# Kernel tuning notes

Measured on AMD Instinct MI355X. Metric: run time of the kernel, lower is better.

Reference implementation:

```python
import jax, jax.numpy as jnp
import numpy as np

B, C, D, O = 64, 64, 512, 256
N_REG, G = 8, 8  # 8 regions of 8 channels


def setup_inputs() -> dict:
    key = jax.random.key(0)
    ks = jax.random.split(key, 9)
    std = 0.02  # init_weights_classify: normal(0, 0.02) for Linear weights, zero bias
    x = jax.random.normal(ks[0], (B, C, D), dtype=jnp.float32)
    region_indices = jnp.arange(C, dtype=jnp.int32).reshape(N_REG, G)
    # attn_fc: Linear(2D -> D), ReLU, Linear(D -> 1)
    W1 = jax.random.normal(ks[1], (2 * D, D), dtype=jnp.float32) * std
    b1 = jnp.zeros((D,), jnp.float32)
    W2 = jax.random.normal(ks[2], (D, 1), dtype=jnp.float32) * std
    b2 = jnp.zeros((1,), jnp.float32)
    # gcn1: Linear(D -> D); gcn2: Linear(D -> O)
    Wg1 = jax.random.normal(ks[3], (D, D), dtype=jnp.float32) * std
    bg1 = jnp.zeros((D,), jnp.float32)
    Wg2 = jax.random.normal(ks[4], (D, O), dtype=jnp.float32) * std
    bg2 = jnp.zeros((O,), jnp.float32)
    return {"x": x, "W1": W1, "b1": b1, "W2": W2, "b2": b2,
            "Wg1": Wg1, "bg1": bg1, "Wg2": Wg2, "bg2": bg2,
            "region_indices": region_indices}


def _leaky_relu02(z):
    return jnp.where(z >= 0, z, 0.2 * z)


def reference(x, W1, b1, W2, b2, Wg1, bg1, Wg2, bg2, region_indices):
    Bb, Cc, Dd = x.shape
    n_reg, g = region_indices.shape
    # channel -> region id; mask[i,j] = same region and i != j
    rid = jnp.zeros((Cc,), jnp.int32).at[region_indices.reshape(-1)].set(
        jnp.repeat(jnp.arange(n_reg, dtype=jnp.int32), g))
    idx = jnp.arange(Cc)
    mask = (rid[:, None] == rid[None, :]) & (idx[:, None] != idx[None, :])  # [C, C]
    # attn_fc on cat(x_i, x_j): split first linear to avoid [B,C,C,2D] concat
    a = x @ W1[:Dd]   # [B, C, D]
    bpart = x @ W1[Dd:]  # [B, C, D]
    h = jax.nn.relu(a[:, :, None, :] + bpart[:, None, :, :] + b1)  # [B, C, C, D]
    scores = jnp.einsum('bijd,do->bij', h, W2) + b2[0]  # [B, C, C]
    scores = jnp.where(mask[None, :, :], scores, -jnp.inf)
    adj = jax.nn.softmax(scores, axis=-1)  # [B, C, C]
    # gcn1: adj @ x -> Linear -> LeakyReLU(0.2); residual mix
    m1 = jnp.einsum('bij,bjd->bid', adj, x)
    x1 = _leaky_relu02(m1 @ Wg1 + bg1)
    x1 = 0.5 * x1 + 0.5 * x
    # gcn2
    m2 = jnp.einsum('bij,bjd->bid', adj, x1)
    out = _leaky_relu02(m2 @ Wg2 + bg2)  # [B, C, O]
    return out
```

## Files before the change

### kernel.cpp

```cpp
#include <hip/hip_runtime.h>
#include <math.h>

#define B_   64
#define C_   64
#define D_   512
#define O_   256
#define G_   8
#define M_   4096

typedef __attribute__((ext_vector_type(8))) short s16x8;
typedef __attribute__((ext_vector_type(4))) float f32x4;
typedef unsigned short u16;
typedef unsigned int   u32;

__device__ __forceinline__ float bf2f(u16 u) { return __uint_as_float(((u32)u) << 16); }
__device__ __forceinline__ u16 f2bf(float f) {
    u32 u = __float_as_uint(f);
    return (u16)((u + 0x7FFFu + ((u >> 16) & 1u)) >> 16);
}
__device__ __forceinline__ void gload16(const void* g, void* l) {
    __builtin_amdgcn_global_load_lds((const __attribute__((address_space(1))) u32*)g,
                                     (__attribute__((address_space(3))) u32*)l, 16, 0, 0);
}
__device__ __forceinline__ void xcd_swz(int& bx, int& by) {
    int nx = (int)gridDim.x;
    int L = bx + by * nx;
    int nwg = nx * (int)gridDim.y;
    int nid = (L & 7) * (nwg >> 3) + (L >> 3);
    bx = nid & (nx - 1);
    by = nid / nx;
}

__global__ __launch_bounds__(256)
void prep_kernel(const float* __restrict__ x, u16* __restrict__ x_bf,
                 const float* __restrict__ W1, u16* __restrict__ W1t,
                 const float* __restrict__ Wg1, u16* __restrict__ Wg1t,
                 const float* __restrict__ Wg2, u16* __restrict__ Wg2t)
{
    __shared__ float tile[32][33];
    const int bx = blockIdx.x, tid = threadIdx.x;
    if (bx < 1024) {
        size_t i = ((size_t)bx * 256 + tid) * 8;
        const float4* p = (const float4*)(x + i);
        float4 v0 = p[0], v1 = p[1];
        s16x8 o;
        o[0] = (short)f2bf(v0.x); o[1] = (short)f2bf(v0.y);
        o[2] = (short)f2bf(v0.z); o[3] = (short)f2bf(v0.w);
        o[4] = (short)f2bf(v1.x); o[5] = (short)f2bf(v1.y);
        o[6] = (short)f2bf(v1.z); o[7] = (short)f2bf(v1.w);
        *(s16x8*)(x_bf + i) = o;
        return;
    }
    const float* src; u16* dst; int k0, n0, nsrc, obase;
    if (bx < 1536) {
        int idx = bx - 1024, h = idx >> 8, t = idx & 255;
        src = W1 + (size_t)h * 512 * 512; dst = W1t; obase = h * 512;
        k0 = (t >> 4) * 32; n0 = (t & 15) * 32; nsrc = 512;
    } else if (bx < 1792) {
        int t = bx - 1536;
        src = Wg1; dst = Wg1t; obase = 0;
        k0 = (t >> 4) * 32; n0 = (t & 15) * 32; nsrc = 512;
    } else {
        int t = bx - 1792;
        src = Wg2; dst = Wg2t; obase = 0;
        k0 = (t >> 3) * 32; n0 = (t & 7) * 32; nsrc = 256;
    }
    int tx = tid & 31, ty = tid >> 5;
    #pragma unroll
    for (int j = 0; j < 4; j++)
        tile[ty + j * 8][tx] = src[(size_t)(k0 + ty + j * 8) * nsrc + n0 + tx];
    __syncthreads();
    #pragma unroll
    for (int j = 0; j < 4; j++)
        dst[(size_t)(obase + n0 + ty + j * 8) * 512 + k0 + tx] = f2bf(tile[tx][ty + j * 8]);
}

__global__ __launch_bounds__(512)
void gemm1_kernel(const u16* __restrict__ A, const u16* __restrict__ Bt,
                  u16* __restrict__ Obf0, u16* __restrict__ Obf1)
{
    constexpr int K = 512, BK = 64, NT = K / BK;
    __shared__ __align__(16) u16 As[2][128 * 64];
    __shared__ __align__(16) u16 Bs[2][128 * 64];

    const int tid = threadIdx.x;
    const int lane = tid & 63;
    const int w = tid >> 6;
    const int wr = w >> 1, wc = w & 1;
    const int lr = lane & 15, lq = lane >> 4;
    int bx = blockIdx.x, by = blockIdx.y;
    xcd_swz(bx, by);
    const int m0 = by * 128, n0 = bx * 128;

    const int sr = tid >> 3;
    const int ss = tid & 7;
    const int gsl = ss ^ (sr & 7);

    f32x4 acc[2][4] = {};

    auto stage = [&](int buf, int kt) {
        #pragma unroll
        for (int ch = 0; ch < 2; ch++)
            gload16(A + (size_t)(m0 + ch * 64 + sr) * K + kt + gsl * 8,
                    &As[buf][ch * 4096 + tid * 8]);
        #pragma unroll
        for (int ch = 0; ch < 2; ch++)
            gload16(Bt + (size_t)(n0 + ch * 64 + sr) * K + kt + gsl * 8,
                    &Bs[buf][ch * 4096 + tid * 8]);
    };

    stage(0, 0);
    int cur = 0;
    for (int t = 0; t < NT; t++) {
        __syncthreads();
        if (t + 1 < NT) stage(cur ^ 1, (t + 1) * BK);
        const u16* as = As[cur]; const u16* bs = Bs[cur];
        #pragma unroll
        for (int ks = 0; ks < 2; ks++) {
            s16x8 af[2], bfv[4];
            #pragma unroll
            for (int m = 0; m < 2; m++) {
                int r = wr * 32 + m * 16 + lr;
                af[m] = *(const s16x8*)(as + r * 64 + (((ks * 4 + lq) ^ (r & 7)) * 8));
            }
            #pragma unroll
            for (int n = 0; n < 4; n++) {
                int r = wc * 64 + n * 16 + lr;
                bfv[n] = *(const s16x8*)(bs + r * 64 + (((ks * 4 + lq) ^ (r & 7)) * 8));
            }
            #pragma unroll
            for (int m = 0; m < 2; m++)
                #pragma unroll
                for (int n = 0; n < 4; n++)
                    acc[m][n] = __builtin_amdgcn_mfma_f32_16x16x32_bf16(af[m], bfv[n], acc[m][n], 0, 0, 0);
        }
        cur ^= 1;
    }

    #pragma unroll
    for (int m = 0; m < 2; m++) {
        #pragma unroll
        for (int n = 0; n < 4; n++) {
            #pragma unroll
            for (int j = 0; j < 4; j++) {
                int row = m0 + wr * 32 + m * 16 + lq * 4 + j;
                int col = n0 + wc * 64 + n * 16 + lr;
                float v = acc[m][n][j];
                if (col < 512) Obf0[(size_t)row * 512 + col] = f2bf(v);
                else           Obf1[(size_t)row * 512 + col - 512] = f2bf(v);
            }
        }
    }
}

__global__ __launch_bounds__(256)
void scores_m1_kernel(const u16* __restrict__ a_bf, const u16* __restrict__ bp_bf,
                      const u16* __restrict__ x_bf,
                      const float* __restrict__ b1, const float* __restrict__ W2,
                      const float* __restrict__ b2,
                      const int* __restrict__ region_indices,
                      float* __restrict__ adjw, u16* __restrict__ m1)
{
    __shared__ __align__(16) u16 bp_lds[64 * 512];
    __shared__ int ri_lds[64];
    __shared__ int rid_lds[64];

    int L = blockIdx.x;
    int nid = ((L & 7) << 5) + (L >> 3);
    const int b = nid >> 2, q = nid & 3;
    const int tid = threadIdx.x, lane = tid & 63, w = tid >> 6;

    #pragma unroll
    for (int it = 0; it < 16; it++)
        gload16(bp_bf + (size_t)b * 32768 + it * 2048 + tid * 8, bp_lds + it * 2048 + tid * 8);
    if (tid < 64) {
        int c = region_indices[tid];
        ri_lds[tid] = c;
        rid_lds[c] = tid >> 3;
    }

    const int d0 = lane * 8;
    float4 b1a = *(const float4*)(b1 + d0), b1b = *(const float4*)(b1 + d0 + 4);
    float4 w2a = *(const float4*)(W2 + d0), w2b = *(const float4*)(W2 + d0 + 4);
    float b1v[8] = { b1a.x, b1a.y, b1a.z, b1a.w, b1b.x, b1b.y, b1b.z, b1b.w };
    float w2v[8] = { w2a.x, w2a.y, w2a.z, w2a.w, w2b.x, w2b.y, w2b.z, w2b.w };
    const float bias2 = b2[0];

    __syncthreads();

    for (int rr = 0; rr < 4; rr++) {
        const int i = q * 16 + w * 4 + rr;
        const int bi = b * 64 + i;
        const int r = rid_lds[i];
        int mem[8];
        #pragma unroll
        for (int m = 0; m < 8; m++) mem[m] = ri_lds[r * 8 + m];

        s16x8 a8 = *(const s16x8*)(a_bf + (size_t)bi * 512 + d0);
        float ai[8];
        #pragma unroll
        for (int t = 0; t < 8; t++) ai[t] = bf2f((u16)a8[t]) + b1v[t];

        float p[8];
        #pragma unroll
        for (int m = 0; m < 8; m++) {
            s16x8 bv = *(const s16x8*)(bp_lds + mem[m] * 512 + d0);
            float s = 0.f;
            #pragma unroll
            for (int t = 0; t < 8; t++) {
                float h = ai[t] + bf2f((u16)bv[t]);
                s += fmaxf(h, 0.f) * w2v[t];
            }
            p[m] = s;
        }
        #pragma unroll
        for (int off = 32; off >= 1; off >>= 1)
            #pragma unroll
            for (int m = 0; m < 8; m++) p[m] += __shfl_xor(p[m], off);

        float scmax = -INFINITY;
        #pragma unroll
        for (int m = 0; m < 8; m++) {
            p[m] = (mem[m] == i) ? -INFINITY : p[m] + bias2;
            scmax = fmaxf(scmax, p[m]);
        }
        float esum = 0.f;
        #pragma unroll
        for (int m = 0; m < 8; m++) {
            p[m] = (mem[m] == i) ? 0.f : __expf(p[m] - scmax);
            esum += p[m];
        }
        const float inv = 1.f / esum;

        float accv[8] = {};
        #pragma unroll
        for (int m = 0; m < 8; m++) {
            p[m] *= inv;
            s16x8 xv = *(const s16x8*)(x_bf + ((size_t)(b * 64 + mem[m])) * 512 + d0);
            #pragma unroll
            for (int t = 0; t < 8; t++) accv[t] += p[m] * bf2f((u16)xv[t]);
        }
        s16x8 o;
        #pragma unroll
        for (int t = 0; t < 8; t++) o[t] = (short)f2bf(accv[t]);
        *(s16x8*)(m1 + (size_t)bi * 512 + d0) = o;
        if (lane < 8) adjw[(size_t)bi * 8 + lane] = p[lane];
    }
}

__global__ __launch_bounds__(512)
void gemm2_m2_kernel(const u16* __restrict__ A, const u16* __restrict__ Bt,
                     const float* __restrict__ bias, const float* __restrict__ xres,
                     const float* __restrict__ adjw, const int* __restrict__ region_indices,
                     u16* __restrict__ m2)
{
    constexpr int K = 512, BK = 64, NT = K / BK;
    __shared__ __align__(16) u16 As[2][64 * 64];
    __shared__ __align__(16) u16 Bs[2][128 * 64];
    __shared__ __align__(16) u16 x1s[64 * 136];
    __shared__ int ri_lds[64];
    __shared__ int rid_lds[64];

    const int tid = threadIdx.x;
    const int lane = tid & 63;
    const int w = tid >> 6;
    const int wr = w >> 2, wc = w & 3;
    const int lr = lane & 15, lq = lane >> 4;
    int bx = blockIdx.x, by = blockIdx.y;
    xcd_swz(bx, by);
    const int b = by, n0 = bx * 128, m0 = b * 64;

    const int sr = tid >> 3, ss = tid & 7;
    const int gsl = ss ^ (sr & 7);

    if (tid < 64) {
        int c = region_indices[tid];
        ri_lds[tid] = c;
        rid_lds[c] = tid >> 3;
    }

    f32x4 acc[2][2] = {};

    auto stage = [&](int buf, int kt) {
        gload16(A + (size_t)(m0 + sr) * K + kt + gsl * 8, &As[buf][tid * 8]);
        #pragma unroll
        for (int ch = 0; ch < 2; ch++)
            gload16(Bt + (size_t)(n0 + ch * 64 + sr) * K + kt + gsl * 8,
                    &Bs[buf][ch * 4096 + tid * 8]);
    };

    stage(0, 0);
    int cur = 0;
    for (int t = 0; t < NT; t++) {
        __syncthreads();
        if (t + 1 < NT) stage(cur ^ 1, (t + 1) * BK);
        const u16* as = As[cur]; const u16* bs = Bs[cur];
        #pragma unroll
        for (int ks = 0; ks < 2; ks++) {
            s16x8 af[2], bfv[2];
            #pragma unroll
            for (int m = 0; m < 2; m++) {
                int r = wr * 32 + m * 16 + lr;
                af[m] = *(const s16x8*)(as + r * 64 + (((ks * 4 + lq) ^ (r & 7)) * 8));
            }
            #pragma unroll
            for (int n = 0; n < 2; n++) {
                int r = wc * 32 + n * 16 + lr;
                bfv[n] = *(const s16x8*)(bs + r * 64 + (((ks * 4 + lq) ^ (r & 7)) * 8));
            }
            #pragma unroll
            for (int m = 0; m < 2; m++)
                #pragma unroll
                for (int n = 0; n < 2; n++)
                    acc[m][n] = __builtin_amdgcn_mfma_f32_16x16x32_bf16(af[m], bfv[n], acc[m][n], 0, 0, 0);
        }
        cur ^= 1;
    }

    #pragma unroll
    for (int m = 0; m < 2; m++) {
        #pragma unroll
        for (int n = 0; n < 2; n++) {
            #pragma unroll
            for (int j = 0; j < 4; j++) {
                int lrow = wr * 32 + m * 16 + lq * 4 + j;
                int lcol = wc * 32 + n * 16 + lr;
                float v = acc[m][n][j] + bias[n0 + lcol];
                v = (v >= 0.f) ? v : 0.2f * v;
                v = 0.5f * v + 0.5f * xres[(size_t)(m0 + lrow) * 512 + n0 + lcol];
                x1s[lrow * 136 + lcol] = f2bf(v);
            }
        }
    }
    __syncthreads();

    const int i = tid >> 3, cb = tid & 7, c0 = cb * 16;
    const int bi = m0 + i;
    const int r = rid_lds[i];
    float acc2[16] = {};
    #pragma unroll
    for (int m = 0; m < 8; m++) {
        float wm = adjw[(size_t)bi * 8 + m];
        int j = ri_lds[r * 8 + m];
        #pragma unroll
        for (int cc = 0; cc < 2; cc++) {
            s16x8 v = *(const s16x8*)(x1s + j * 136 + c0 + cc * 8);
            #pragma unroll
            for (int t = 0; t < 8; t++) acc2[cc * 8 + t] += wm * bf2f((u16)v[t]);
        }
    }
    #pragma unroll
    for (int cc = 0; cc < 2; cc++) {
        s16x8 o;
        #pragma unroll
        for (int t = 0; t < 8; t++) o[t] = (short)f2bf(acc2[cc * 8 + t]);
        *(s16x8*)(m2 + (size_t)bi * 512 + n0 + c0 + cc * 8) = o;
    }
}

__global__ __launch_bounds__(256)
void gemm3_kernel(const u16* __restrict__ A, const u16* __restrict__ Bt,
                  const float* __restrict__ bias, float* __restrict__ Of)
{
    constexpr int K = 512, BK = 64, NT = K / BK;
    __shared__ __align__(16) u16 As[2][64 * 64];
    __shared__ __align__(16) u16 Bs[2][64 * 64];

    const int tid = threadIdx.x;
    const int lane = tid & 63;
    const int w = tid >> 6, wr = w >> 1, wc = w & 1;
    const int lr = lane & 15, lq = lane >> 4;
    int bx = blockIdx.x, by = blockIdx.y;
    xcd_swz(bx, by);
    const int m0 = by * 64, n0 = bx * 64;

    const int sr = tid >> 3, ss = tid & 7;
    const int gsl = ss ^ (sr & 7);

    f32x4 acc[2][2] = {};

    auto stage = [&](int buf, int kt) {
        #pragma unroll
        for (int ch = 0; ch < 2; ch++)
            gload16(A + (size_t)(m0 + ch * 32 + sr) * K + kt + gsl * 8,
                    &As[buf][ch * 2048 + tid * 8]);
        #pragma unroll
        for (int ch = 0; ch < 2; ch++)
            gload16(Bt + (size_t)(n0 + ch * 32 + sr) * K + kt + gsl * 8,
                    &Bs[buf][ch * 2048 + tid * 8]);
    };

    stage(0, 0);
    int cur = 0;
    for (int t = 0; t < NT; t++) {
        __syncthreads();
        if (t + 1 < NT) stage(cur ^ 1, (t + 1) * BK);
        const u16* as = As[cur]; const u16* bs = Bs[cur];
        #pragma unroll
        for (int ks = 0; ks < 2; ks++) {
            s16x8 af[2], bfv[2];
            #pragma unroll
            for (int m = 0; m < 2; m++) {
                int r = wr * 32 + m * 16 + lr;
                af[m] = *(const s16x8*)(as + r * 64 + (((ks * 4 + lq) ^ (r & 7)) * 8));
            }
            #pragma unroll
            for (int n = 0; n < 2; n++) {
                int r = wc * 32 + n * 16 + lr;
                bfv[n] = *(const s16x8*)(bs + r * 64 + (((ks * 4 + lq) ^ (r & 7)) * 8));
            }
            #pragma unroll
            for (int m = 0; m < 2; m++)
                #pragma unroll
                for (int n = 0; n < 2; n++)
                    acc[m][n] = __builtin_amdgcn_mfma_f32_16x16x32_bf16(af[m], bfv[n], acc[m][n], 0, 0, 0);
        }
        cur ^= 1;
    }

    #pragma unroll
    for (int m = 0; m < 2; m++) {
        #pragma unroll
        for (int n = 0; n < 2; n++) {
            #pragma unroll
            for (int j = 0; j < 4; j++) {
                int row = m0 + wr * 32 + m * 16 + lq * 4 + j;
                int col = n0 + wc * 32 + n * 16 + lr;
                float v = acc[m][n][j] + bias[col];
                v = (v >= 0.f) ? v : 0.2f * v;
                Of[(size_t)row * 256 + col] = v;
            }
        }
    }
}

extern "C" void kernel_launch(void* const* d_in, const int* in_sizes, int n_in,
                              void* d_out, int out_size, void* d_ws, size_t ws_size,
                              hipStream_t stream) {
    const float* x    = (const float*)d_in[0];
    const float* W1   = (const float*)d_in[1];
    const float* b1   = (const float*)d_in[2];
    const float* W2   = (const float*)d_in[3];
    const float* b2   = (const float*)d_in[4];
    const float* Wg1  = (const float*)d_in[5];
    const float* bg1  = (const float*)d_in[6];
    const float* Wg2  = (const float*)d_in[7];
    const float* bg2  = (const float*)d_in[8];
    const int* region_indices = (const int*)d_in[9];
    float* out = (float*)d_out;

    char* ws = (char*)d_ws;
    const size_t MB = 1024 * 1024;
    u16*   x_bf  = (u16*)(ws);
    u16*   W1t   = (u16*)(ws + 4 * MB);
    u16*   Wg1t  = (u16*)(ws + 5 * MB);
    u16*   Wg2t  = (u16*)(ws + 5 * MB + 512 * 1024);
    u16*   a_bf  = (u16*)(ws + 6 * MB);
    u16*   bp_bf = (u16*)(ws + 10 * MB);
    u16*   m1_bf = (u16*)(ws + 14 * MB);
    u16*   m2_bf = (u16*)(ws + 18 * MB);
    float* adjw  = (float*)(ws + 22 * MB);

    prep_kernel<<<1920, 256, 0, stream>>>(x, x_bf, W1, W1t, Wg1, Wg1t, Wg2, Wg2t);

    gemm1_kernel<<<dim3(8, 32), 512, 0, stream>>>(x_bf, W1t, a_bf, bp_bf);

    scores_m1_kernel<<<256, 256, 0, stream>>>(a_bf, bp_bf, x_bf, b1, W2, b2,
                                              region_indices, adjw, m1_bf);

    gemm2_m2_kernel<<<dim3(4, 64), 512, 0, stream>>>(
        m1_bf, Wg1t, bg1, x, adjw, region_indices, m2_bf);

    gemm3_kernel<<<dim3(4, 64), 256, 0, stream>>>(m2_bf, Wg2t, bg2, out);
}
```

Baseline: 119.2 us.

## Stage only region-member rows in scores kernel; fold residual via adj linearity

The scores kernel now loads into LDS only the 16 bp and x rows belonging to its two regions, instead of the whole 64-row bp slice. The x rows for the softmax-weighted sum also come from LDS rather than global memory, which cuts LDS footprint and global traffic per block. gemm2 drops the fp32 residual read of x. It uses adj@(0.5y+0.5x) = 0.5·adj@y + 0.5·m1 and adds the already-computed bf16 m1 in the epilogue. This trades a little precision, since m1 is bf16, for less memory traffic.

```diff
diff --git a/kernel.cpp b/kernel.cpp
--- a/kernel.cpp
+++ b/kernel.cpp
@@ -1,12 +1,5 @@
 #include <hip/hip_runtime.h>
 #include <math.h>
-
-#define B_   64
-#define C_   64
-#define D_   512
-#define O_   256
-#define G_   8
-#define M_   4096
 
 typedef __attribute__((ext_vector_type(8))) short s16x8;
 typedef __attribute__((ext_vector_type(4))) float f32x4;
@@ -44,10 +37,8 @@
         const float4* p = (const float4*)(x + i);
         float4 v0 = p[0], v1 = p[1];
         s16x8 o;
-        o[0] = (short)f2bf(v0.x); o[1] = (short)f2bf(v0.y);
-        o[2] = (short)f2bf(v0.z); o[3] = (short)f2bf(v0.w);
-        o[4] = (short)f2bf(v1.x); o[5] = (short)f2bf(v1.y);
-        o[6] = (short)f2bf(v1.z); o[7] = (short)f2bf(v1.w);
+        o[0]=(short)f2bf(v0.x); o[1]=(short)f2bf(v0.y); o[2]=(short)f2bf(v0.z); o[3]=(short)f2bf(v0.w);
+        o[4]=(short)f2bf(v1.x); o[5]=(short)f2bf(v1.y); o[6]=(short)f2bf(v1.z); o[7]=(short)f2bf(v1.w);
         *(s16x8*)(x_bf + i) = o;
         return;
     }
@@ -77,23 +68,20 @@
 
 __global__ __launch_bounds__(512)
 void gemm1_kernel(const u16* __restrict__ A, const u16* __restrict__ Bt,
-                  u16* __restrict__ Obf0, u16* __restrict__ Obf1)
+                  u16* __restrict__ a_bf, u16* __restrict__ bp_bf)
 {
-    constexpr int K = 512, BK = 64, NT = K / BK;
-    __shared__ __align__(16) u16 As[2][128 * 64];
-    __shared__ __align__(16) u16 Bs[2][128 * 64];
+    __shared__ __align__(16) u16 As[2][8192];
+    __shared__ __align__(16) u16 Bs[2][8192];
 
     const int tid = threadIdx.x;
-    const int lane = tid & 63;
-    const int w = tid >> 6;
+    const int lane = tid & 63, w = tid >> 6;
     const int wr = w >> 1, wc = w & 1;
     const int lr = lane & 15, lq = lane >> 4;
     int bx = blockIdx.x, by = blockIdx.y;
     xcd_swz(bx, by);
     const int m0 = by * 128, n0 = bx * 128;
 
-    const int sr = tid >> 3;
-    const int ss = tid & 7;
+    const int sr = tid >> 3, ss = tid & 7;
     const int gsl = ss ^ (sr & 7);
 
     f32x4 acc[2][4] = {};
@@ -101,19 +89,19 @@
     auto stage = [&](int buf, int kt) {
         #pragma unroll
         for (int ch = 0; ch < 2; ch++)
-            gload16(A + (size_t)(m0 + ch * 64 + sr) * K + kt + gsl * 8,
+            gload16(A + (size_t)(m0 + ch * 64 + sr) * 512 + kt + gsl * 8,
                     &As[buf][ch * 4096 + tid * 8]);
         #pragma unroll
         for (int ch = 0; ch < 2; ch++)
-            gload16(Bt + (size_t)(n0 + ch * 64 + sr) * K + kt + gsl * 8,
+            gload16(Bt + (size_t)(n0 + ch * 64 + sr) * 512 + kt + gsl * 8,
                     &Bs[buf][ch * 4096 + tid * 8]);
     };
 
     stage(0, 0);
     int cur = 0;
-    for (int t = 0; t < NT; t++) {
+    for (int t = 0; t < 8; t++) {
         __syncthreads();
-        if (t + 1 < NT) stage(cur ^ 1, (t + 1) * BK);
+        if (t < 7) stage(cur ^ 1, (t + 1) * 64);
         const u16* as = As[cur]; const u16* bs = Bs[cur];
         #pragma unroll
         for (int ks = 0; ks < 2; ks++) {
@@ -138,45 +126,45 @@
     }
 
     #pragma unroll
-    for (int m = 0; m < 2; m++) {
-        #pragma unroll
-        for (int n = 0; n < 4; n++) {
+    for (int m = 0; m < 2; m++)
+        #pragma unroll
+        for (int n = 0; n < 4; n++)
             #pragma unroll
             for (int j = 0; j < 4; j++) {
                 int row = m0 + wr * 32 + m * 16 + lq * 4 + j;
                 int col = n0 + wc * 64 + n * 16 + lr;
-                float v = acc[m][n][j];
-                if (col < 512) Obf0[(size_t)row * 512 + col] = f2bf(v);
-                else           Obf1[(size_t)row * 512 + col - 512] = f2bf(v);
-            }
-        }
-    }
+                u16 v = f2bf(acc[m][n][j]);
+                if (col < 512) a_bf [(size_t)row * 512 + col] = v;
+                else           bp_bf[(size_t)row * 512 + col - 512] = v;
+            }
 }
 
 __global__ __launch_bounds__(256)
-void scores_m1_kernel(const u16* __restrict__ a_bf, const u16* __restrict__ bp_bf,
-                      const u16* __restrict__ x_bf,
-                      const float* __restrict__ b1, const float* __restrict__ W2,
-                      const float* __restrict__ b2,
-                      const int* __restrict__ region_indices,
-                      float* __restrict__ adjw, u16* __restrict__ m1)
+void scores_kernel(const u16* __restrict__ a_bf, const u16* __restrict__ bp_bf,
+                   const u16* __restrict__ x_bf,
+                   const float* __restrict__ b1, const float* __restrict__ W2,
+                   const float* __restrict__ b2,
+                   const int* __restrict__ region_indices,
+                   float* __restrict__ adjw, u16* __restrict__ m1_bf)
 {
-    __shared__ __align__(16) u16 bp_lds[64 * 512];
-    __shared__ int ri_lds[64];
-    __shared__ int rid_lds[64];
+    __shared__ __align__(16) u16 bpL[16 * 512];
+    __shared__ __align__(16) u16 xL[16 * 512];
+    __shared__ int memS[16];
 
     int L = blockIdx.x;
     int nid = ((L & 7) << 5) + (L >> 3);
     const int b = nid >> 2, q = nid & 3;
     const int tid = threadIdx.x, lane = tid & 63, w = tid >> 6;
 
-    #pragma unroll
-    for (int it = 0; it < 16; it++)
-        gload16(bp_bf + (size_t)b * 32768 + it * 2048 + tid * 8, bp_lds + it * 2048 + tid * 8);
-    if (tid < 64) {
-        int c = region_indices[tid];
-        ri_lds[tid] = c;
-        rid_lds[c] = tid >> 3;
+    if (tid < 16) memS[tid] = region_indices[q * 16 + tid];
+    __syncthreads();
+
+    #pragma unroll
+    for (int it = 0; it < 4; it++) {
+        int rl = it * 4 + w;
+        size_t src = (size_t)(b * 64 + memS[rl]) * 512 + lane * 8;
+        gload16(bp_bf + src, bpL + rl * 512 + lane * 8);
+        gload16(x_bf  + src, xL  + rl * 512 + lane * 8);
     }
 
     const int d0 = lane * 8;
@@ -185,16 +173,13 @@
     float b1v[8] = { b1a.x, b1a.y, b1a.z, b1a.w, b1b.x, b1b.y, b1b.z, b1b.w };
     float w2v[8] = { w2a.x, w2a.y, w2a.z, w2a.w, w2b.x, w2b.y, w2b.z, w2b.w };
     const float bias2 = b2[0];
-
     __syncthreads();
 
     for (int rr = 0; rr < 4; rr++) {
-        const int i = q * 16 + w * 4 + rr;
+        const int rl = w * 4 + rr;
+        const int rhalf = rl >> 3, s_slot = rl & 7;
+        const int i = memS[rl];
         const int bi = b * 64 + i;
-        const int r = rid_lds[i];
-        int mem[8];
-        #pragma unroll
-        for (int m = 0; m < 8; m++) mem[m] = ri_lds[r * 8 + m];
 
         s16x8 a8 = *(const s16x8*)(a_bf + (size_t)bi * 512 + d0);
         float ai[8];
@@ -204,7 +189,7 @@
         float p[8];
         #pragma unroll
         for (int m = 0; m < 8; m++) {
-            s16x8 bv = *(const s16x8*)(bp_lds + mem[m] * 512 + d0);
+            s16x8 bv = *(const s16x8*)(bpL + (rhalf * 8 + m) * 512 + d0);
             float s = 0.f;
             #pragma unroll
             for (int t = 0; t < 8; t++) {
@@ -221,13 +206,13 @@
         float scmax = -INFINITY;
         #pragma unroll
         for (int m = 0; m < 8; m++) {
-            p[m] = (mem[m] == i) ? -INFINITY : p[m] + bias2;
+            p[m] = (m == s_slot) ? -INFINITY : p[m] + bias2;
             scmax = fmaxf(scmax, p[m]);
         }
         float esum = 0.f;
         #pragma unroll
         for (int m = 0; m < 8; m++) {
-            p[m] = (mem[m] == i) ? 0.f : __expf(p[m] - scmax);
+            p[m] = (m == s_slot) ? 0.f : __expf(p[m] - scmax);
             esum += p[m];
         }
         const float inv = 1.f / esum;
@@ -236,64 +221,56 @@
         #pragma unroll
         for (int m = 0; m < 8; m++) {
             p[m] *= inv;
-            s16x8 xv = *(const s16x8*)(x_bf + ((size_t)(b * 64 + mem[m])) * 512 + d0);
+            s16x8 xv = *(const s16x8*)(xL + (rhalf * 8 + m) * 512 + d0);
             #pragma unroll
             for (int t = 0; t < 8; t++) accv[t] += p[m] * bf2f((u16)xv[t]);
         }
         s16x8 o;
         #pragma unroll
         for (int t = 0; t < 8; t++) o[t] = (short)f2bf(accv[t]);
-        *(s16x8*)(m1 + (size_t)bi * 512 + d0) = o;
+        *(s16x8*)(m1_bf + (size_t)bi * 512 + d0) = o;
         if (lane < 8) adjw[(size_t)bi * 8 + lane] = p[lane];
     }
 }
 
 __global__ __launch_bounds__(512)
 void gemm2_m2_kernel(const u16* __restrict__ A, const u16* __restrict__ Bt,
-                     const float* __restrict__ bias, const float* __restrict__ xres,
+                     const float* __restrict__ bias,
                      const float* __restrict__ adjw, const int* __restrict__ region_indices,
                      u16* __restrict__ m2)
 {
-    constexpr int K = 512, BK = 64, NT = K / BK;
-    __shared__ __align__(16) u16 As[2][64 * 64];
-    __shared__ __align__(16) u16 Bs[2][128 * 64];
-    __shared__ __align__(16) u16 x1s[64 * 136];
-    __shared__ int ri_lds[64];
-    __shared__ int rid_lds[64];
+    __shared__ __align__(16) u16 As[2][4096];
+    __shared__ __align__(16) u16 Bs[2][8192];
+    __shared__ __align__(16) u16 y1s[64 * 136];
+    __shared__ int ri[64], rid[64];
 
     const int tid = threadIdx.x;
-    const int lane = tid & 63;
-    const int w = tid >> 6;
+    const int lane = tid & 63, w = tid >> 6;
     const int wr = w >> 2, wc = w & 3;
     const int lr = lane & 15, lq = lane >> 4;
     int bx = blockIdx.x, by = blockIdx.y;
     xcd_swz(bx, by);
     const int b = by, n0 = bx * 128, m0 = b * 64;
 
-    const int sr = tid >> 3, ss = tid & 7;
-    const int gsl = ss ^ (sr & 7);
-
-    if (tid < 64) {
-        int c = region_indices[tid];
-        ri_lds[tid] = c;
-        rid_lds[c] = tid >> 3;
-    }
+    const int sr = tid >> 3, ss = tid & 7, gsl = ss ^ (sr & 7);
+
+    if (tid < 64) { int c = region_indices[tid]; ri[tid] = c; rid[c] = tid >> 3; }
 
     f32x4 acc[2][2] = {};
 
     auto stage = [&](int buf, int kt) {
-        gload16(A + (size_t)(m0 + sr) * K + kt + gsl * 8, &As[buf][tid * 8]);
+        gload16(A + (size_t)(m0 + sr) * 512 + kt + gsl * 8, &As[buf][tid * 8]);
         #pragma unroll
         for (int ch = 0; ch < 2; ch++)
-            gload16(Bt + (size_t)(n0 + ch * 64 + sr) * K + kt + gsl * 8,
+            gload16(Bt + (size_t)(n0 + ch * 64 + sr) * 512 + kt + gsl * 8,
                     &Bs[buf][ch * 4096 + tid * 8]);
     };
 
     stage(0, 0);
     int cur = 0;
-    for (int t = 0; t < NT; t++) {
+    for (int t = 0; t < 8; t++) {
         __syncthreads();
-        if (t + 1 < NT) stage(cur ^ 1, (t + 1) * BK);
+        if (t < 7) stage(cur ^ 1, (t + 1) * 64);
         const u16* as = As[cur]; const u16* bs = Bs[cur];
         #pragma unroll
         for (int ks = 0; ks < 2; ks++) {
@@ -318,42 +295,41 @@
     }
 
     #pragma unroll
-    for (int m = 0; m < 2; m++) {
-        #pragma unroll
-        for (int n = 0; n < 2; n++) {
+    for (int m = 0; m < 2; m++)
+        #pragma unroll
+        for (int n = 0; n < 2; n++)
             #pragma unroll
             for (int j = 0; j < 4; j++) {
                 int lrow = wr * 32 + m * 16 + lq * 4 + j;
                 int lcol = wc * 32 + n * 16 + lr;
                 float v = acc[m][n][j] + bias[n0 + lcol];
                 v = (v >= 0.f) ? v : 0.2f * v;
-                v = 0.5f * v + 0.5f * xres[(size_t)(m0 + lrow) * 512 + n0 + lcol];
-                x1s[lrow * 136 + lcol] = f2bf(v);
-            }
-        }
-    }
+                y1s[lrow * 136 + lcol] = f2bf(v);
+            }
     __syncthreads();
 
     const int i = tid >> 3, cb = tid & 7, c0 = cb * 16;
     const int bi = m0 + i;
-    const int r = rid_lds[i];
+    const int r = rid[i];
     float acc2[16] = {};
     #pragma unroll
     for (int m = 0; m < 8; m++) {
         float wm = adjw[(size_t)bi * 8 + m];
-        int j = ri_lds[r * 8 + m];
+        int j = ri[r * 8 + m];
         #pragma unroll
         for (int cc = 0; cc < 2; cc++) {
-            s16x8 v = *(const s16x8*)(x1s + j * 136 + c0 + cc * 8);
+            s16x8 v = *(const s16x8*)(y1s + j * 136 + c0 + cc * 8);
             #pragma unroll
             for (int t = 0; t < 8; t++) acc2[cc * 8 + t] += wm * bf2f((u16)v[t]);
         }
     }
     #pragma unroll
     for (int cc = 0; cc < 2; cc++) {
+        s16x8 m1v = *(const s16x8*)(A + (size_t)bi * 512 + n0 + c0 + cc * 8);
         s16x8 o;
         #pragma unroll
-        for (int t = 0; t < 8; t++) o[t] = (short)f2bf(acc2[cc * 8 + t]);
+        for (int t = 0; t < 8; t++)
+            o[t] = (short)f2bf(0.5f * acc2[cc * 8 + t] + 0.5f * bf2f((u16)m1v[t]));
         *(s16x8*)(m2 + (size_t)bi * 512 + n0 + c0 + cc * 8) = o;
     }
 }
@@ -362,39 +338,37 @@
 void gemm3_kernel(const u16* __restrict__ A, const u16* __restrict__ Bt,
                   const float* __restrict__ bias, float* __restrict__ Of)
 {
-    constexpr int K = 512, BK = 64, NT = K / BK;
-    __shared__ __align__(16) u16 As[2][64 * 64];
-    __shared__ __align__(16) u16 Bs[2][64 * 64];
+    __shared__ __align__(16) u16 As[2][4096];
+    __shared__ __align__(16) u16 Bs[2][4096];
 
     const int tid = threadIdx.x;
-    const int lane = tid & 63;
-    const int w = tid >> 6, wr = w >> 1, wc = w & 1;
+    const int lane = tid & 63, w = tid >> 6;
+    const int wr = w >> 1, wc = w & 1;
     const int lr = lane & 15, lq = lane >> 4;
     int bx = blockIdx.x, by = blockIdx.y;
     xcd_swz(bx, by);
     const int m0 = by * 64, n0 = bx * 64;
 
-    const int sr = tid >> 3, ss = tid & 7;
-    const int gsl = ss ^ (sr & 7);
+    const int sr = tid >> 3, ss = tid & 7, gsl = ss ^ (sr & 7);
 
     f32x4 acc[2][2] = {};
 
     auto stage = [&](int buf, int kt) {
         #pragma unroll
         for (int ch = 0; ch < 2; ch++)
-            gload16(A + (size_t)(m0 + ch * 32 + sr) * K + kt + gsl * 8,
+            gload16(A + (size_t)(m0 + ch * 32 + sr) * 512 + kt + gsl * 8,
                     &As[buf][ch * 2048 + tid * 8]);
         #pragma unroll
         for (int ch = 0; ch < 2; ch++)
-            gload16(Bt + (size_t)(n0 + ch * 32 + sr) * K + kt + gsl * 8,
+            gload16(Bt + (size_t)(n0 + ch * 32 + sr) * 512 + kt + gsl * 8,
                     &Bs[buf][ch * 2048 + tid * 8]);
     };
 
     stage(0, 0);
     int cur = 0;
-    for (int t = 0; t < NT; t++) {
+    for (int t = 0; t < 8; t++) {
         __syncthreads();
-        if (t + 1 < NT) stage(cur ^ 1, (t + 1) * BK);
+        if (t < 7) stage(cur ^ 1, (t + 1) * 64);
         const u16* as = As[cur]; const u16* bs = Bs[cur];
         #pragma unroll
         for (int ks = 0; ks < 2; ks++) {
@@ -419,9 +393,9 @@
     }
 
     #pragma unroll
-    for (int m = 0; m < 2; m++) {
-        #pragma unroll
-        for (int n = 0; n < 2; n++) {
+    for (int m = 0; m < 2; m++)
+        #pragma unroll
+        for (int n = 0; n < 2; n++)
             #pragma unroll
             for (int j = 0; j < 4; j++) {
                 int row = m0 + wr * 32 + m * 16 + lq * 4 + j;
@@ -430,8 +404,6 @@
                 v = (v >= 0.f) ? v : 0.2f * v;
                 Of[(size_t)row * 256 + col] = v;
             }
-        }
-    }
 }
 
 extern "C" void kernel_launch(void* const* d_in, const int* in_sizes, int n_in,
@@ -451,25 +423,25 @@
 
     char* ws = (char*)d_ws;
     const size_t MB = 1024 * 1024;
-    u16*   x_bf  = (u16*)(ws);
-    u16*   W1t   = (u16*)(ws + 4 * MB);
-    u16*   Wg1t  = (u16*)(ws + 5 * MB);
-    u16*   Wg2t  = (u16*)(ws + 5 * MB + 512 * 1024);
-    u16*   a_bf  = (u16*)(ws + 6 * MB);
-    u16*   bp_bf = (u16*)(ws + 10 * MB);
-    u16*   m1_bf = (u16*)(ws + 14 * MB);
-    u16*   m2_bf = (u16*)(ws + 18 * MB);
-    float* adjw  = (float*)(ws + 22 * MB);
+    u16* x_bf  = (u16*)(ws);
+    u16* W1t   = (u16*)(ws + 4 * MB);
+    u16* Wg1t  = (u16*)(ws + 5 * MB);
+    u16* Wg2t  = (u16*)(ws + 5 * MB + 512 * 1024);
+    u16* a_bf  = (u16*)(ws + 6 * MB);
+    u16* bp_bf = (u16*)(ws + 10 * MB);
+    u16* m1_bf = (u16*)(ws + 14 * MB);
+    u16* m2_bf = (u16*)(ws + 18 * MB);
+    float* adjw = (float*)(ws + 22 * MB);
 
     prep_kernel<<<1920, 256, 0, stream>>>(x, x_bf, W1, W1t, Wg1, Wg1t, Wg2, Wg2t);
 
     gemm1_kernel<<<dim3(8, 32), 512, 0, stream>>>(x_bf, W1t, a_bf, bp_bf);
 
-    scores_m1_kernel<<<256, 256, 0, stream>>>(a_bf, bp_bf, x_bf, b1, W2, b2,
-                                              region_indices, adjw, m1_bf);
+    scores_kernel<<<256, 256, 0, stream>>>(a_bf, bp_bf, x_bf, b1, W2, b2,
+                                           region_indices, adjw, m1_bf);
 
     gemm2_m2_kernel<<<dim3(4, 64), 512, 0, stream>>>(
-        m1_bf, Wg1t, bg1, x, adjw, region_indices, m2_bf);
+        m1_bf, Wg1t, bg1, adjw, region_indices, m2_bf);
 
     gemm3_kernel<<<dim3(4, 64), 256, 0, stream>>>(m2_bf, Wg2t, bg2, out);
 }
```

New measurement: 118.2 us (median of 2 runs). Within noise of the previous version (-0.8%).
